# Optimization experiments

Measured on AMD Instinct MI355X. Metric: run time of the kernel, lower is better.

The kernel has to match this reference:

```python
import jax, jax.numpy as jnp
import numpy as np

# spconv.SparseConv4d(C_in, 16, (1,3,3,3), stride=1, padding=0) on spatial_shape [1000,1000,40]:
# leading kernel dim is size 1, so this is a regular (non-submanifold) 3D sparse conv,
# valid padding -> output spatial shape (998, 998, 38). Implemented as gather-GEMM-scatter:
# input point p contributes feat(p) @ W[k] to output coord p - offset[k] for each of 27 taps.

N = 200000
C_IN = 64
C_OUT = 16
K = 3
OUT_SP = (998, 998, 38)  # 1000-3+1, 1000-3+1, 40-3+1
SENT = OUT_SP[0] * OUT_SP[1] * OUT_SP[2]  # sentinel linear index for invalid taps


def setup_inputs() -> dict:
    key = jax.random.key(0)
    k1, k2, k3, k4, k5, k6 = jax.random.split(key, 6)
    feats = jax.random.normal(k1, (N, C_IN), dtype=jnp.float32)
    x = jax.random.randint(k2, (N,), 0, 1000, dtype=jnp.int32)
    y = jax.random.randint(k3, (N,), 0, 1000, dtype=jnp.int32)
    z = jax.random.randint(k4, (N,), 0, 40, dtype=jnp.int32)
    coords = jnp.stack([jnp.zeros((N,), jnp.int32), x, y, z], axis=1)  # [N,4] (b,x,y,z)
    fan_in = C_IN * K * K * K
    W = jax.random.normal(k5, (K * K * K, C_IN, C_OUT), dtype=jnp.float32) / np.sqrt(fan_in)
    bias = jax.random.normal(k6, (C_OUT,), dtype=jnp.float32) * 0.01
    return {"input": feats, "coords": coords, "W": W, "bias": bias}


def reference(input, coords, W, bias):
    # kernel tap offsets, C-order over (kx,ky,kz) in [0,3)^3 -> [27,3]
    off = jnp.stack(
        jnp.meshgrid(jnp.arange(K), jnp.arange(K), jnp.arange(K), indexing="ij"),
        axis=-1,
    ).reshape(K * K * K, 3).astype(jnp.int32)
    xyz = coords[:, 1:4]                              # [N,3]
    oc = xyz[:, None, :] - off[None, :, :]            # [N,27,3] output coord per tap
    out_sp = jnp.array(OUT_SP, dtype=jnp.int32)
    valid = jnp.all((oc >= 0) & (oc < out_sp), axis=-1)  # [N,27]
    lin = oc[..., 0] * (OUT_SP[1] * OUT_SP[2]) + oc[..., 1] * OUT_SP[2] + oc[..., 2]
    lin = jnp.where(valid, lin, SENT).reshape(-1)     # [N*27]

    # gather-GEMM: per-tap GEMM over all active voxels
    contrib = jnp.einsum("nc,kco->nko", input, W)     # [N,27,16]
    contrib = jnp.where(valid[..., None], contrib, 0.0).reshape(-1, C_OUT)

    NK = N * (K * K * K)
    uniq, inv = jnp.unique(lin, return_inverse=True, size=NK, fill_value=SENT)
    inv = inv.reshape(-1)
    # scatter-add into unique output sites
    out = jax.ops.segment_sum(contrib, inv, num_segments=NK)  # [NK,16]
    cnt = jax.ops.segment_sum(valid.reshape(-1).astype(jnp.int32), inv, num_segments=NK)
    out = out + jnp.where(cnt[:, None] > 0, bias[None, :], 0.0)
    return out, uniq
```

## Files before the change

kernel.cpp:

```cpp
#include <hip/hip_runtime.h>

#define N_PTS   200000
#define CIN     64
#define COUT    16
#define KK      27
#define SXD     998
#define SYD     998
#define SZD     38
#define STRX    (SYD*SZD)
#define SENTV   (SXD*SYD*SZD)
#define NKTOT   (N_PTS*KK)
#define NWORDS  ((SENTV+31)/32)
#define NCHUNK  ((NWORDS+255)/256)
#define NB      16000

typedef float f32x4 __attribute__((ext_vector_type(4)));

__global__ void mark_kernel(const int* __restrict__ coords, unsigned* __restrict__ bm,
                            unsigned* __restrict__ mu, unsigned* __restrict__ hist) {
    int n = blockIdx.x * blockDim.x + threadIdx.x;
    if (n >= N_PTS) return;
    int4 c = ((const int4*)coords)[n];
    int x = c.y, y = c.z, z = c.w;
    if (hist) {
        unsigned key = ((unsigned)x >> 3) * 128u + ((unsigned)y >> 3);
        atomicAdd(&hist[key], 1u);
    }
    int zlo = z - 2; if (zlo < 0) zlo = 0;
    int zhi = z;     if (zhi > SZD - 1) zhi = SZD - 1;
    unsigned nb = (unsigned)(zhi - zlo + 1);
    unsigned mseed = (1u << nb) - 1u;
    #pragma unroll
    for (int dx = 0; dx < 3; dx++) {
        int ox = x - dx;
        if (ox < 0 || ox >= SXD) continue;
        #pragma unroll
        for (int dy = 0; dy < 3; dy++) {
            int oy = y - dy;
            if (oy < 0 || oy >= SYD) continue;
            int lin = ox*STRX + oy*SZD + zlo;
            unsigned w = (unsigned)lin >> 5;
            unsigned b = (unsigned)lin & 31u;
            unsigned lowm = mseed << b;
            unsigned old = atomicOr(&bm[w], lowm);
            unsigned col = old & lowm;
            if (col) atomicOr(&mu[w], col);
            if (b + nb > 32u) {
                unsigned highm = mseed >> (32u - b);
                unsigned old2 = atomicOr(&bm[w+1], highm);
                unsigned col2 = old2 & highm;
                if (col2) atomicOr(&mu[w+1], col2);
            }
        }
    }
}

__global__ void chunk_sums_kernel(const unsigned* __restrict__ bm, unsigned* __restrict__ csums) {
    int w = blockIdx.x * 256 + threadIdx.x;
    unsigned c = (w < NWORDS) ? (unsigned)__popc(bm[w]) : 0u;
    __shared__ unsigned s[256];
    s[threadIdx.x] = c;
    __syncthreads();
    for (int off = 128; off > 0; off >>= 1) {
        if (threadIdx.x < off) s[threadIdx.x] += s[threadIdx.x + off];
        __syncthreads();
    }
    if (threadIdx.x == 0) csums[blockIdx.x] = s[0];
}

__global__ void scan_all_kernel(const unsigned* __restrict__ csums,
                                unsigned* __restrict__ cprefix,
                                unsigned* __restrict__ Uptr,
                                const unsigned* __restrict__ hist,
                                unsigned* __restrict__ bpos,
                                int do_buckets) {
    __shared__ unsigned s[256];
    __shared__ unsigned run_s;
    if (blockIdx.x == 1 && !do_buckets) return;
    const unsigned* src = (blockIdx.x == 0) ? csums : hist;
    unsigned* dst       = (blockIdx.x == 0) ? cprefix : bpos;
    int count           = (blockIdx.x == 0) ? NCHUNK : NB;
    if (threadIdx.x == 0) run_s = 0;
    __syncthreads();
    for (int base = 0; base < count; base += 256) {
        int i = base + threadIdx.x;
        unsigned v = (i < count) ? src[i] : 0u;
        s[threadIdx.x] = v;
        __syncthreads();
        for (int off = 1; off < 256; off <<= 1) {
            unsigned t = (threadIdx.x >= off) ? s[threadIdx.x - off] : 0u;
            __syncthreads();
            s[threadIdx.x] += t;
            __syncthreads();
        }
        unsigned run = run_s;
        if (i < count) dst[i] = run + s[threadIdx.x] - v;
        unsigned tile_total = s[255];
        __syncthreads();
        if (threadIdx.x == 255) run_s = run + tile_total;
        __syncthreads();
    }
    if (blockIdx.x == 0 && threadIdx.x == 0) Uptr[0] = run_s;
}

__global__ void word_prefix_kernel(const unsigned* __restrict__ bm,
                                   const unsigned* __restrict__ cprefix,
                                   unsigned* __restrict__ wp) {
    int w = blockIdx.x * 256 + threadIdx.x;
    unsigned v = (w < NWORDS) ? (unsigned)__popc(bm[w]) : 0u;
    __shared__ unsigned s[256];
    s[threadIdx.x] = v;
    __syncthreads();
    for (int off = 1; off < 256; off <<= 1) {
        unsigned t = (threadIdx.x >= off) ? s[threadIdx.x - off] : 0u;
        __syncthreads();
        s[threadIdx.x] += t;
        __syncthreads();
    }
    if (w < NWORDS) wp[w] = cprefix[blockIdx.x] + s[threadIdx.x] - v;
}

__global__ void pidx_kernel(const int* __restrict__ coords, unsigned* __restrict__ bpos,
                            int4* __restrict__ csorted) {
    int n = blockIdx.x * blockDim.x + threadIdx.x;
    if (n >= N_PTS) return;
    int4 c = ((const int4*)coords)[n];
    unsigned key = ((unsigned)c.y >> 3) * 128u + ((unsigned)c.z >> 3);
    unsigned pos = atomicAdd(&bpos[key], 1u);
    csorted[pos] = make_int4(n, c.y, c.z, c.w);
}

__global__ void fill_out_kernel(float* __restrict__ out, const float* __restrict__ bias,
                                const unsigned* __restrict__ Uptr) {
    unsigned U = Uptr[0];
    unsigned i = blockIdx.x * blockDim.x + threadIdx.x;
    if (i >= (unsigned)NKTOT * 4u) return;
    unsigned row = i >> 2;
    int q = i & 3;
    float4 v;
    if (row < U) v = ((const float4*)bias)[q];
    else         v = make_float4(0.f, 0.f, 0.f, 0.f);
    ((float4*)out)[i] = v;
}

__global__ void fill_uniq_kernel(float* __restrict__ uniq) {
    unsigned i = blockIdx.x * blockDim.x + threadIdx.x;
    if (i < (unsigned)NKTOT) uniq[i] = (float)SENTV;
}

__global__ void tail_kernel(float* __restrict__ out, float* __restrict__ uniq,
                            const unsigned* __restrict__ Uptr) {
    unsigned U = Uptr[0];
    unsigned i = blockIdx.x * blockDim.x + threadIdx.x;
    if (i >= (unsigned)NKTOT || i < U) return;
    f32x4 z4 = {0.f, 0.f, 0.f, 0.f};
    f32x4* dst = (f32x4*)(out + (size_t)i * COUT);
    #pragma unroll
    for (int q = 0; q < 4; q++) __builtin_nontemporal_store(z4, dst + q);
    __builtin_nontemporal_store((float)SENTV, uniq + i);
}

template<bool DO_BIAS>
__global__ void write_uniq_kernel(const unsigned* __restrict__ bm,
                                  const unsigned* __restrict__ mu,
                                  const unsigned* __restrict__ wp,
                                  const unsigned* __restrict__ Uptr,
                                  float* __restrict__ uniq,
                                  float* __restrict__ out,
                                  const float* __restrict__ bias) {
    __shared__ float sbuf[8192];
    unsigned U = Uptr[0];
    int wfirst = blockIdx.x * 256;
    int wnext  = wfirst + 256;
    unsigned r0 = wp[wfirst];
    unsigned r1 = (wnext < NWORDS) ? wp[wnext] : U;
    int w = wfirst + threadIdx.x;
    unsigned bits = 0, r = 0, mbits = 0;
    if (w < NWORDS) {
        bits = bm[w];
        r    = wp[w];
        if (DO_BIAS) mbits = mu[w];
    }
    unsigned bb = bits, rr = r;
    while (bb) {
        int b = __ffs(bb) - 1;
        bb &= bb - 1;
        sbuf[rr - r0] = (float)((unsigned)w * 32u + b);
        rr++;
    }
    __syncthreads();
    unsigned span = r1 - r0;
    for (unsigned j = threadIdx.x; j < span; j += 256)
        __builtin_nontemporal_store(sbuf[j], uniq + r0 + j);
    if (DO_BIAS && bits && mbits) {
        f32x4 bv[4];
        #pragma unroll
        for (int q = 0; q < 4; q++) bv[q] = ((const f32x4*)bias)[q];
        bb = bits; rr = r;
        while (bb) {
            int b = __ffs(bb) - 1;
            bb &= bb - 1;
            if ((mbits >> b) & 1u) {
                f32x4* dst = (f32x4*)(out + (size_t)rr * COUT);
                #pragma unroll
                for (int q = 0; q < 4; q++) __builtin_nontemporal_store(bv[q], dst + q);
            }
            rr++;
        }
    }
}

template<bool SORTED>
__launch_bounds__(256)
__global__ void scatter_mm_kernel(const float* __restrict__ feats,
                                  const int4* __restrict__ cpts,
                                  const float* __restrict__ W,
                                  const float* __restrict__ bias,
                                  const unsigned* __restrict__ bm,
                                  const unsigned* __restrict__ mu,
                                  const unsigned* __restrict__ wp,
                                  float* __restrict__ out) {
    int i = blockIdx.x * 256 + threadIdx.x;
    if (i >= N_PTS) return;
    int4 cc = cpts[i];
    int n = SORTED ? cc.x : i;
    int x = cc.y, y = cc.z, z = cc.w;

    int zlo = z - 2; if (zlo < 0) zlo = 0;

    unsigned bmv[9], muv[9], mu2v[9], wpv[9], b0v[9];
    bool valv[9];
    #pragma unroll
    for (int dx = 0; dx < 3; dx++) {
        int ox = x - dx;
        #pragma unroll
        for (int dy = 0; dy < 3; dy++) {
            int k = dx*3 + dy;
            int oy = y - dy;
            bool v = (ox >= 0) & (ox < SXD) & (oy >= 0) & (oy < SYD);
            valv[k] = v;
            unsigned lin0 = (unsigned)(ox*STRX + oy*SZD + zlo);
            unsigned w0 = v ? (lin0 >> 5) : 0u;
            b0v[k] = lin0 & 31u;
            bmv[k]  = v ? bm[w0] : 0u;
            muv[k]  = v ? mu[w0] : 0u;
            mu2v[k] = (v && (lin0 & 31u) >= 30u) ? mu[w0 + 1] : 0u;
            wpv[k]  = v ? wp[w0] : 0u;
        }
    }

    f32x4 f[CIN/4];
    const f32x4* fin4 = (const f32x4*)(feats + (size_t)n * CIN);
    #pragma unroll
    for (int q = 0; q < CIN/4; q++) f[q] = fin4[q];

    f32x4 bv[4];
    #pragma unroll
    for (int q = 0; q < 4; q++) bv[q] = ((const f32x4*)bias)[q];

    #pragma unroll 1
    for (int dx = 0; dx < 3; dx++) {
        #pragma unroll 1
        for (int dy = 0; dy < 3; dy++) {
            int k = dx*3 + dy;
            if (!valv[k]) continue;
            unsigned b0 = b0v[k];
            unsigned r0 = wpv[k] + (unsigned)__popc(bmv[k] & ((1u << b0) - 1u));
            unsigned mlo = muv[k], mhi = mu2v[k];
            #pragma unroll
            for (int dz = 0; dz < 3; dz++) {
                int oz = z - dz;
                if (oz < 0 || oz >= SZD) continue;
                unsigned j = (unsigned)(oz - zlo);
                unsigned bb = b0 + j;
                bool ismul = (((bb < 32u) ? (mlo >> bb) : (mhi >> (bb - 32u))) & 1u) != 0u;
                unsigned rank = r0 + j;

                const float* wk = W + (size_t)(dx*9 + dy*3 + dz) * (CIN*COUT);
                float acc[COUT];
                #pragma unroll
                for (int o = 0; o < COUT; o++) acc[o] = 0.f;
                #pragma unroll
                for (int c4 = 0; c4 < CIN/4; c4++) {
                    f32x4 fv = f[c4];
                    const float* wrow = wk + c4 * 4 * COUT;
                    #pragma unroll
                    for (int o = 0; o < COUT; o++) {
                        acc[o] += fv.x * wrow[o] + fv.y * wrow[COUT + o]
                                + fv.z * wrow[2*COUT + o] + fv.w * wrow[3*COUT + o];
                    }
                }

                float* dst = out + (size_t)rank * COUT;
                if (!ismul) {
                    #pragma unroll
                    for (int q = 0; q < 4; q++) {
                        f32x4 vv;
                        vv.x = acc[q*4+0] + bv[q].x;
                        vv.y = acc[q*4+1] + bv[q].y;
                        vv.z = acc[q*4+2] + bv[q].z;
                        vv.w = acc[q*4+3] + bv[q].w;
                        ((f32x4*)dst)[q] = vv;
                    }
                } else {
                    #pragma unroll
                    for (int o = 0; o < COUT; o++) atomicAdd(dst + o, acc[o]);
                }
            }
        }
    }
}

extern "C" void kernel_launch(void* const* d_in, const int* in_sizes, int n_in,
                              void* d_out, int out_size, void* d_ws, size_t ws_size,
                              hipStream_t stream) {
    const float* feats  = (const float*)d_in[0];
    const int*   coords = (const int*)d_in[1];
    const float* W      = (const float*)d_in[2];
    const float* bias   = (const float*)d_in[3];
    float* out  = (float*)d_out;
    float* uniq = out + (size_t)NKTOT * COUT;

    unsigned* ws = (unsigned*)d_ws;

    size_t o_bm      = 0;
    size_t o_mu      = o_bm + NWORDS;
    size_t o_hist    = o_mu + NWORDS;
    size_t o_wp      = o_hist + NB;
    size_t o_bpos    = o_wp + NWORDS;
    size_t o_csums   = o_bpos + NB;
    size_t o_cprefix = o_csums + NCHUNK;
    size_t o_Uptr    = o_cprefix + NCHUNK;
    size_t o_csort   = (o_Uptr + 1 + 3) & ~(size_t)3;
    size_t fast_words = o_csort + 4 * (size_t)N_PTS;

    if (ws_size >= fast_words * sizeof(unsigned)) {
        unsigned* bm      = ws + o_bm;
        unsigned* mu      = ws + o_mu;
        unsigned* hist    = ws + o_hist;
        unsigned* wp      = ws + o_wp;
        unsigned* bpos    = ws + o_bpos;
        unsigned* csums   = ws + o_csums;
        unsigned* cprefix = ws + o_cprefix;
        unsigned* Uptr    = ws + o_Uptr;
        int4*     csorted = (int4*)(ws + o_csort);

        hipMemsetAsync(bm, 0, (2 * (size_t)NWORDS + NB) * sizeof(unsigned), stream);
        mark_kernel<<<(N_PTS + 255) / 256, 256, 0, stream>>>(coords, bm, mu, hist);
        chunk_sums_kernel<<<NCHUNK, 256, 0, stream>>>(bm, csums);
        scan_all_kernel<<<2, 256, 0, stream>>>(csums, cprefix, Uptr, hist, bpos, 1);
        pidx_kernel<<<(N_PTS + 255) / 256, 256, 0, stream>>>(coords, bpos, csorted);
        word_prefix_kernel<<<NCHUNK, 256, 0, stream>>>(bm, cprefix, wp);
        write_uniq_kernel<true><<<NCHUNK, 256, 0, stream>>>(
            bm, mu, wp, Uptr, uniq, out, bias);
        tail_kernel<<<(NKTOT + 255) / 256, 256, 0, stream>>>(out, uniq, Uptr);
        scatter_mm_kernel<true><<<(N_PTS + 255) / 256, 256, 0, stream>>>(
            feats, csorted, W, bias, bm, mu, wp, out);
    } else {
        unsigned* bm      = ws;
        unsigned* wp      = ws + NWORDS;
        unsigned* csums   = ws + 2 * (size_t)NWORDS;
        unsigned* cprefix = csums + NCHUNK;
        unsigned* Uptr    = cprefix + NCHUNK;

        hipMemsetAsync(bm, 0, (size_t)NWORDS * sizeof(unsigned), stream);
        mark_kernel<<<(N_PTS + 255) / 256, 256, 0, stream>>>(coords, bm, bm, nullptr);
        chunk_sums_kernel<<<NCHUNK, 256, 0, stream>>>(bm, csums);
        scan_all_kernel<<<2, 256, 0, stream>>>(csums, cprefix, Uptr, nullptr, nullptr, 0);
        word_prefix_kernel<<<NCHUNK, 256, 0, stream>>>(bm, cprefix, wp);
        fill_out_kernel<<<(NKTOT * 4 + 255) / 256, 256, 0, stream>>>(out, bias, Uptr);
        fill_uniq_kernel<<<(NKTOT + 255) / 256, 256, 0, stream>>>(uniq);
        write_uniq_kernel<false><<<NCHUNK, 256, 0, stream>>>(
            bm, bm, wp, Uptr, uniq, out, bias);
        scatter_mm_kernel<false><<<(N_PTS + 255) / 256, 256, 0, stream>>>(
            feats, (const int4*)coords, W, bias, bm, bm, wp, out);
    }
}
```

Before: 1.472 ms.

## Sort points before marking, swizzle block order, load bitmap words lazily

Points are now bucket-sorted by spatial key before the bitmap-marking pass, so the atomicOr traffic hits nearby words from each block. Both the mark kernel and the scatter-GEMM kernel use an XCD-aware block swizzle, so consecutive sorted chunks land on the same die and share its L2. The scatter kernel no longer preloads 9 sets of bitmap, multiplicity and prefix words into registers; it loads them per tap and adds an occupancy hint to cut register pressure. The scan is split into separate single-block launches, which adds kernel launches and serialises the histogram and scatter steps ahead of marking.

New measurement: 1.745 ms. +18.5%, slower.

```diff
diff --git a/kernel.cpp b/kernel.cpp
--- a/kernel.cpp
+++ b/kernel.cpp
@@ -13,19 +13,66 @@
 #define NWORDS  ((SENTV+31)/32)
 #define NCHUNK  ((NWORDS+255)/256)
 #define NB      16000
+#define NBLK_PTS 784
 
 typedef float f32x4 __attribute__((ext_vector_type(4)));
 
-__global__ void mark_kernel(const int* __restrict__ coords, unsigned* __restrict__ bm,
-                            unsigned* __restrict__ mu, unsigned* __restrict__ hist) {
+__device__ __forceinline__ int swz_lin(unsigned bid, unsigned nblk) {
+    unsigned per = nblk >> 3;
+    return (int)((bid & 7u) * per + (bid >> 3));
+}
+
+__global__ void hist_kernel(const int* __restrict__ coords, unsigned* __restrict__ hist) {
     int n = blockIdx.x * blockDim.x + threadIdx.x;
     if (n >= N_PTS) return;
     int4 c = ((const int4*)coords)[n];
+    unsigned key = ((unsigned)c.y >> 3) * 128u + ((unsigned)c.z >> 3);
+    atomicAdd(&hist[key], 1u);
+}
+
+__global__ void scan1_kernel(const unsigned* __restrict__ src, unsigned* __restrict__ dst,
+                             int count, unsigned* __restrict__ Uptr) {
+    __shared__ unsigned s[256];
+    __shared__ unsigned run_s;
+    if (threadIdx.x == 0) run_s = 0;
+    __syncthreads();
+    for (int base = 0; base < count; base += 256) {
+        int i = base + threadIdx.x;
+        unsigned v = (i < count) ? src[i] : 0u;
+        s[threadIdx.x] = v;
+        __syncthreads();
+        for (int off = 1; off < 256; off <<= 1) {
+            unsigned t = (threadIdx.x >= off) ? s[threadIdx.x - off] : 0u;
+            __syncthreads();
+            s[threadIdx.x] += t;
+            __syncthreads();
+        }
+        unsigned run = run_s;
+        if (i < count) dst[i] = run + s[threadIdx.x] - v;
+        unsigned tile_total = s[255];
+        __syncthreads();
+        if (threadIdx.x == 255) run_s = run + tile_total;
+        __syncthreads();
+    }
+    if (Uptr && threadIdx.x == 0) Uptr[0] = run_s;
+}
+
+__global__ void pidx_kernel(const int* __restrict__ coords, unsigned* __restrict__ bpos,
+                            int4* __restrict__ csorted) {
+    int n = blockIdx.x * blockDim.x + threadIdx.x;
+    if (n >= N_PTS) return;
+    int4 c = ((const int4*)coords)[n];
+    unsigned key = ((unsigned)c.y >> 3) * 128u + ((unsigned)c.z >> 3);
+    unsigned pos = atomicAdd(&bpos[key], 1u);
+    csorted[pos] = make_int4(n, c.y, c.z, c.w);
+}
+
+__global__ void mark_sorted_kernel(const int4* __restrict__ cpts, unsigned* __restrict__ bm,
+                                   unsigned* __restrict__ mu) {
+    int i = swz_lin(blockIdx.x, gridDim.x) * 256 + (int)threadIdx.x;
+    if (i >= N_PTS) return;
+    int4 c = cpts[i];
     int x = c.y, y = c.z, z = c.w;
-    if (hist) {
-        unsigned key = ((unsigned)x >> 3) * 128u + ((unsigned)y >> 3);
-        atomicAdd(&hist[key], 1u);
-    }
     int zlo = z - 2; if (zlo < 0) zlo = 0;
     int zhi = z;     if (zhi > SZD - 1) zhi = SZD - 1;
     unsigned nb = (unsigned)(zhi - zlo + 1);
@@ -55,6 +102,41 @@
     }
 }
 
+__global__ void mark_raw_kernel(const int* __restrict__ coords, unsigned* __restrict__ bm,
+                                unsigned* __restrict__ mu) {
+    int n = blockIdx.x * blockDim.x + threadIdx.x;
+    if (n >= N_PTS) return;
+    int4 c = ((const int4*)coords)[n];
+    int x = c.y, y = c.z, z = c.w;
+    int zlo = z - 2; if (zlo < 0) zlo = 0;
+    int zhi = z;     if (zhi > SZD - 1) zhi = SZD - 1;
+    unsigned nb = (unsigned)(zhi - zlo + 1);
+    unsigned mseed = (1u << nb) - 1u;
+    #pragma unroll
+    for (int dx = 0; dx < 3; dx++) {
+        int ox = x - dx;
+        if (ox < 0 || ox >= SXD) continue;
+        #pragma unroll
+        for (int dy = 0; dy < 3; dy++) {
+            int oy = y - dy;
+            if (oy < 0 || oy >= SYD) continue;
+            int lin = ox*STRX + oy*SZD + zlo;
+            unsigned w = (unsigned)lin >> 5;
+            unsigned b = (unsigned)lin & 31u;
+            unsigned lowm = mseed << b;
+            unsigned old = atomicOr(&bm[w], lowm);
+            unsigned col = old & lowm;
+            if (col) atomicOr(&mu[w], col);
+            if (b + nb > 32u) {
+                unsigned highm = mseed >> (32u - b);
+                unsigned old2 = atomicOr(&bm[w+1], highm);
+                unsigned col2 = old2 & highm;
+                if (col2) atomicOr(&mu[w+1], col2);
+            }
+        }
+    }
+}
+
 __global__ void chunk_sums_kernel(const unsigned* __restrict__ bm, unsigned* __restrict__ csums) {
     int w = blockIdx.x * 256 + threadIdx.x;
     unsigned c = (w < NWORDS) ? (unsigned)__popc(bm[w]) : 0u;
@@ -66,41 +148,6 @@
         __syncthreads();
     }
     if (threadIdx.x == 0) csums[blockIdx.x] = s[0];
-}
-
-__global__ void scan_all_kernel(const unsigned* __restrict__ csums,
-                                unsigned* __restrict__ cprefix,
-                                unsigned* __restrict__ Uptr,
-                                const unsigned* __restrict__ hist,
-                                unsigned* __restrict__ bpos,
-                                int do_buckets) {
-    __shared__ unsigned s[256];
-    __shared__ unsigned run_s;
-    if (blockIdx.x == 1 && !do_buckets) return;
-    const unsigned* src = (blockIdx.x == 0) ? csums : hist;
-    unsigned* dst       = (blockIdx.x == 0) ? cprefix : bpos;
-    int count           = (blockIdx.x == 0) ? NCHUNK : NB;
-    if (threadIdx.x == 0) run_s = 0;
-    __syncthreads();
-    for (int base = 0; base < count; base += 256) {
-        int i = base + threadIdx.x;
-        unsigned v = (i < count) ? src[i] : 0u;
-        s[threadIdx.x] = v;
-        __syncthreads();
-        for (int off = 1; off < 256; off <<= 1) {
-            unsigned t = (threadIdx.x >= off) ? s[threadIdx.x - off] : 0u;
-            __syncthreads();
-            s[threadIdx.x] += t;
-            __syncthreads();
-        }
-        unsigned run = run_s;
-        if (i < count) dst[i] = run + s[threadIdx.x] - v;
-        unsigned tile_total = s[255];
-        __syncthreads();
-        if (threadIdx.x == 255) run_s = run + tile_total;
-        __syncthreads();
-    }
-    if (blockIdx.x == 0 && threadIdx.x == 0) Uptr[0] = run_s;
 }
 
 __global__ void word_prefix_kernel(const unsigned* __restrict__ bm,
@@ -118,16 +165,6 @@
         __syncthreads();
     }
     if (w < NWORDS) wp[w] = cprefix[blockIdx.x] + s[threadIdx.x] - v;
-}
-
-__global__ void pidx_kernel(const int* __restrict__ coords, unsigned* __restrict__ bpos,
-                            int4* __restrict__ csorted) {
-    int n = blockIdx.x * blockDim.x + threadIdx.x;
-    if (n >= N_PTS) return;
-    int4 c = ((const int4*)coords)[n];
-    unsigned key = ((unsigned)c.y >> 3) * 128u + ((unsigned)c.z >> 3);
-    unsigned pos = atomicAdd(&bpos[key], 1u);
-    csorted[pos] = make_int4(n, c.y, c.z, c.w);
 }
 
 __global__ void fill_out_kernel(float* __restrict__ out, const float* __restrict__ bias,
@@ -211,7 +248,7 @@
 }
 
 template<bool SORTED>
-__launch_bounds__(256)
+__launch_bounds__(256, 4)
 __global__ void scatter_mm_kernel(const float* __restrict__ feats,
                                   const int4* __restrict__ cpts,
                                   const float* __restrict__ W,
@@ -220,34 +257,12 @@
                                   const unsigned* __restrict__ mu,
                                   const unsigned* __restrict__ wp,
                                   float* __restrict__ out) {
-    int i = blockIdx.x * 256 + threadIdx.x;
+    int i = swz_lin(blockIdx.x, gridDim.x) * 256 + (int)threadIdx.x;
     if (i >= N_PTS) return;
     int4 cc = cpts[i];
     int n = SORTED ? cc.x : i;
     int x = cc.y, y = cc.z, z = cc.w;
-
     int zlo = z - 2; if (zlo < 0) zlo = 0;
-
-    unsigned bmv[9], muv[9], mu2v[9], wpv[9], b0v[9];
-    bool valv[9];
-    #pragma unroll
-    for (int dx = 0; dx < 3; dx++) {
-        int ox = x - dx;
-        #pragma unroll
-        for (int dy = 0; dy < 3; dy++) {
-            int k = dx*3 + dy;
-            int oy = y - dy;
-            bool v = (ox >= 0) & (ox < SXD) & (oy >= 0) & (oy < SYD);
-            valv[k] = v;
-            unsigned lin0 = (unsigned)(ox*STRX + oy*SZD + zlo);
-            unsigned w0 = v ? (lin0 >> 5) : 0u;
-            b0v[k] = lin0 & 31u;
-            bmv[k]  = v ? bm[w0] : 0u;
-            muv[k]  = v ? mu[w0] : 0u;
-            mu2v[k] = (v && (lin0 & 31u) >= 30u) ? mu[w0 + 1] : 0u;
-            wpv[k]  = v ? wp[w0] : 0u;
-        }
-    }
 
     f32x4 f[CIN/4];
     const f32x4* fin4 = (const f32x4*)(feats + (size_t)n * CIN);
@@ -260,13 +275,18 @@
 
     #pragma unroll 1
     for (int dx = 0; dx < 3; dx++) {
+        int ox = x - dx;
+        if (ox < 0 || ox >= SXD) continue;
         #pragma unroll 1
         for (int dy = 0; dy < 3; dy++) {
-            int k = dx*3 + dy;
-            if (!valv[k]) continue;
-            unsigned b0 = b0v[k];
-            unsigned r0 = wpv[k] + (unsigned)__popc(bmv[k] & ((1u << b0) - 1u));
-            unsigned mlo = muv[k], mhi = mu2v[k];
+            int oy = y - dy;
+            if (oy < 0 || oy >= SYD) continue;
+            unsigned lin0 = (unsigned)(ox*STRX + oy*SZD + zlo);
+            unsigned w0 = lin0 >> 5, b0 = lin0 & 31u;
+            unsigned bmw = bm[w0];
+            unsigned r0  = wp[w0] + (unsigned)__popc(bmw & ((1u << b0) - 1u));
+            unsigned mlo = mu[w0];
+            unsigned mhi = (b0 >= 30u) ? mu[w0 + 1] : 0u;
             #pragma unroll
             for (int dz = 0; dz < 3; dz++) {
                 int oz = z - dz;
@@ -346,15 +366,17 @@
         int4*     csorted = (int4*)(ws + o_csort);
 
         hipMemsetAsync(bm, 0, (2 * (size_t)NWORDS + NB) * sizeof(unsigned), stream);
-        mark_kernel<<<(N_PTS + 255) / 256, 256, 0, stream>>>(coords, bm, mu, hist);
+        hist_kernel<<<(N_PTS + 255) / 256, 256, 0, stream>>>(coords, hist);
+        scan1_kernel<<<1, 256, 0, stream>>>(hist, bpos, NB, nullptr);
+        pidx_kernel<<<(N_PTS + 255) / 256, 256, 0, stream>>>(coords, bpos, csorted);
+        mark_sorted_kernel<<<NBLK_PTS, 256, 0, stream>>>(csorted, bm, mu);
         chunk_sums_kernel<<<NCHUNK, 256, 0, stream>>>(bm, csums);
-        scan_all_kernel<<<2, 256, 0, stream>>>(csums, cprefix, Uptr, hist, bpos, 1);
-        pidx_kernel<<<(N_PTS + 255) / 256, 256, 0, stream>>>(coords, bpos, csorted);
+        scan1_kernel<<<1, 256, 0, stream>>>(csums, cprefix, NCHUNK, Uptr);
         word_prefix_kernel<<<NCHUNK, 256, 0, stream>>>(bm, cprefix, wp);
         write_uniq_kernel<true><<<NCHUNK, 256, 0, stream>>>(
             bm, mu, wp, Uptr, uniq, out, bias);
         tail_kernel<<<(NKTOT + 255) / 256, 256, 0, stream>>>(out, uniq, Uptr);
-        scatter_mm_kernel<true><<<(N_PTS + 255) / 256, 256, 0, stream>>>(
+        scatter_mm_kernel<true><<<NBLK_PTS, 256, 0, stream>>>(
             feats, csorted, W, bias, bm, mu, wp, out);
     } else {
         unsigned* bm      = ws;
@@ -364,15 +386,15 @@
         unsigned* Uptr    = cprefix + NCHUNK;
 
         hipMemsetAsync(bm, 0, (size_t)NWORDS * sizeof(unsigned), stream);
-        mark_kernel<<<(N_PTS + 255) / 256, 256, 0, stream>>>(coords, bm, bm, nullptr);
+        mark_raw_kernel<<<(N_PTS + 255) / 256, 256, 0, stream>>>(coords, bm, bm);
         chunk_sums_kernel<<<NCHUNK, 256, 0, stream>>>(bm, csums);
-        scan_all_kernel<<<2, 256, 0, stream>>>(csums, cprefix, Uptr, nullptr, nullptr, 0);
+        scan1_kernel<<<1, 256, 0, stream>>>(csums, cprefix, NCHUNK, Uptr);
         word_prefix_kernel<<<NCHUNK, 256, 0, stream>>>(bm, cprefix, wp);
         fill_out_kernel<<<(NKTOT * 4 + 255) / 256, 256, 0, stream>>>(out, bias, Uptr);
         fill_uniq_kernel<<<(NKTOT + 255) / 256, 256, 0, stream>>>(uniq);
         write_uniq_kernel<false><<<NCHUNK, 256, 0, stream>>>(
             bm, bm, wp, Uptr, uniq, out, bias);
-        scatter_mm_kernel<false><<<(N_PTS + 255) / 256, 256, 0, stream>>>(
+        scatter_mm_kernel<false><<<NBLK_PTS, 256, 0, stream>>>(
             feats, (const int4*)coords, W, bias, bm, bm, wp, out);
     }
 }
```
